# Optimization experiments

Measured on AMD Instinct MI355X. Metric: run time of the kernel, lower is better.

Reference implementation:

```python
import jax, jax.numpy as jnp
import numpy as np

MIN_HAIRPIN = 4
BIG = 1e30  # stand-in for the numpy reference's 1e18 INF (fp32-safe)


def _dp_single(e_pair, e_unp, allowed):
    """Nussinov min-energy DP for one sequence.
    e_pair: (L,L) f32, e_unp: (L,) f32, allowed: (L,L) bool.
    Returns dp (L,L) and ptr (L,L) backpointers matching the numpy reference:
      0 -> i unpaired, 1 -> j unpaired, 2 -> (i,j) paired, k+3 -> bifurcation at k.
    Vectorised over the antidiagonal (all i for a fixed span s at once).
    """
    L = e_unp.shape[0]
    idx = jnp.arange(L)
    dp0 = jnp.full((L, L), BIG, dtype=e_pair.dtype).at[idx, idx].set(e_unp)
    ptr0 = jnp.full((L, L), -1, dtype=jnp.int32).at[idx, idx].set(0)
    t = jnp.arange(L - 1)  # bifurcation offset k = i + t

    def step(carry, s):
        dp, ptr = carry
        j = idx + s - 1
        valid = j < L
        jc = jnp.minimum(j, L - 1)
        ip1 = jnp.minimum(idx + 1, L - 1)
        jm1 = jnp.maximum(jc - 1, 0)
        opt0 = dp[ip1, jc] + e_unp            # i unpaired
        opt1 = dp[idx, jm1] + e_unp[jc]       # j unpaired
        inner = jnp.where(s >= 3, dp[ip1, jm1], 0.0)
        pair_ok = allowed[idx, jc] & (s - 1 > MIN_HAIRPIN)  # j - i = s - 1
        opt2 = jnp.where(pair_ok, inner + e_pair[idx, jc], BIG)
        k = jnp.minimum(idx[:, None] + t[None, :], L - 1)
        bif = dp[idx[:, None], k] + dp[jnp.minimum(k + 1, L - 1), jc[:, None]]
        bif = jnp.where(t[None, :] < s - 1, bif, BIG)
        cand = jnp.concatenate([opt0[:, None], opt1[:, None], opt2[:, None], bif], axis=1)
        c = jnp.argmin(cand, axis=1)  # first-occurrence argmin == strict-< tie-break
        best = jnp.take_along_axis(cand, c[:, None], axis=1)[:, 0]
        new_ptr = jnp.where(c < 3, c, c + idx).astype(jnp.int32)  # c-3 is offset t -> k+3 = c+i
        dp = dp.at[idx, jc].set(jnp.where(valid, best, dp[idx, jc]))
        ptr = ptr.at[idx, jc].set(jnp.where(valid, new_ptr, ptr[idx, jc]))
        return (dp, ptr), None

    (dp, ptr), _ = jax.lax.scan(step, (dp0, ptr0), jnp.arange(2, L + 1))
    return dp, ptr


def _traceback(ptr):
    """Stack-based traceback of the backpointer matrix. Returns pairs (L,) int32, -1 = unpaired."""
    L = ptr.shape[0]

    def cond(st):
        return st[2] > 0

    def body(st):
        si, sj, sp, res = st
        top = sp - 1
        i, j = si[top], sj[top]
        skip = i >= j
        p = ptr[i, j]
        is0, is1, is2, isk = p == 0, p == 1, p == 2, p >= 3
        k = p - 3
        p1i = jnp.where(is0 | is2, i + 1, i)
        p1j = jnp.where(is1 | is2, j - 1, jnp.where(isk, k, j))
        v1 = (~skip) & jnp.where(is2, i + 1 <= j - 1, True)
        v2 = (~skip) & isk  # bifurcation pushes a second interval (k+1, j)
        res = jnp.where(is2 & (~skip), res.at[i].set(j).at[j].set(i), res)
        si = si.at[top].set(jnp.where(v1, p1i, si[top]))
        sj = sj.at[top].set(jnp.where(v1, p1j, sj[top]))
        slot2 = top + v1.astype(jnp.int32)
        si = si.at[slot2].set(jnp.where(v2, k + 1, si[slot2]))
        sj = sj.at[slot2].set(jnp.where(v2, j, sj[slot2]))
        sp = top + v1.astype(jnp.int32) + v2.astype(jnp.int32)
        return si, sj, sp, res

    si0 = jnp.zeros((L,), jnp.int32)
    sj0 = jnp.zeros((L,), jnp.int32).at[0].set(L - 1)
    res0 = jnp.full((L,), -1, jnp.int32)
    _, _, _, res = jax.lax.while_loop(cond, body, (si0, sj0, jnp.int32(1), res0))
    return res


def _structure_energy(e_pair, e_unp, pairs):
    """E(x,S) = sum_{i unpaired} e_unp[i] + sum_{(i,j) in S, i<j} e_pair[i,j]."""
    L = e_unp.shape[-1]
    clamped = jnp.maximum(pairs, 0)
    unp = jnp.where(pairs < 0, e_unp, 0.0).sum(-1)
    pe = jnp.take_along_axis(e_pair, clamped[..., None], axis=2)[..., 0]
    is_pair = (pairs >= 0) & (jnp.arange(L)[None, :] < clamped)
    return unp + jnp.where(is_pair, pe, 0.0).sum(-1)


def setup_inputs() -> dict:
    key = jax.random.key(0)
    k1, k2, k3 = jax.random.split(key, 3)
    B, L = 32, 384
    e_pair = jax.random.normal(k1, (B, L, L), jnp.float32)
    e_unp = jax.random.normal(k2, (B, L), jnp.float32)
    pair_mask = jax.random.randint(k3, (B, L, L), 0, 2).astype(jnp.bool_)
    return {"e_pair": e_pair, "e_unp": e_unp, "pair_mask": pair_mask}


def reference(e_pair, e_unp, pair_mask):
    dp, ptr = jax.vmap(_dp_single)(e_pair, e_unp, pair_mask)
    pairs = jax.vmap(_traceback)(ptr)  # (B, L) int32, -1 = unpaired
    energy = _structure_energy(e_pair, e_unp, pairs)  # (B,), equals dp[:, 0, -1]
    return pairs, energy
```

## Files before the change

kernel.cpp:

```cpp
#include <hip/hip_runtime.h>

#define LSEQ 384
#define BATCH 32
#define BIGV 1e30f
#define TB_STK 448
#define NN ((size_t)LSEQ * LSEQ)
#define BT 32
#define NT 12
#define PIT 33

__device__ __forceinline__ int detect_mmode_wave(const unsigned char* m0, int lane) {
    unsigned char v = m0[lane & 63];
    unsigned long long big = __ballot(v >= 2);
    unsigned long long off = __ballot((((lane & 63) & 3) != 0) && (v != 0));
    return big ? 2 : (off ? 1 : 0);
}
__device__ __forceinline__ bool mask_read(const void* mask, size_t idx, int mmode) {
    if (mmode == 0) return ((const unsigned int*)mask)[idx] != 0;
    if (mmode == 1) return ((const unsigned char*)mask)[idx] != 0;
    return ((const unsigned short*)mask)[idx] != 0;
}
__device__ __forceinline__ void choice_write(void* mask, size_t idx, int c, int mmode) {
    if (mmode == 0) ((unsigned int*)mask)[idx] = (unsigned int)c;
    else if (mmode == 1) ((unsigned char*)mask)[idx] = (unsigned char)c;
    else ((unsigned short*)mask)[idx] = (unsigned short)c;
}

__device__ __forceinline__ float edge_min32(const float* rowp, const float* colp) {
    float a0 = BIGV, a1 = BIGV, a2 = BIGV, a3 = BIGV;
    #pragma unroll
    for (int kk = 0; kk < 32; kk += 4) {
        float r0 = rowp[kk], r1 = rowp[kk + 1], r2 = rowp[kk + 2], r3 = rowp[kk + 3];
        const float* cb = colp + kk * PIT;
        float c0 = cb[0], c1 = cb[PIT], c2 = cb[2 * PIT], c3 = cb[3 * PIT];
        a0 = fminf(a0, r0 + c0); a1 = fminf(a1, r1 + c1);
        a2 = fminf(a2, r2 + c2); a3 = fminf(a3, r3 + c3);
    }
    return fminf(fminf(a0, a1), fminf(a2, a3));
}

__device__ __forceinline__ void minplus_waves(
    const float* __restrict__ dpG, int I, int J, const int* fm, int nfm,
    int wv, int lane, float part[4][BT][PIT])
{
    const int r0 = (lane >> 3) << 2, c0 = (lane & 7) << 2;
    float r16[16];
    #pragma unroll
    for (int z = 0; z < 16; ++z) r16[z] = BIGV;
    const int mi = wv >> 1, kqB = (wv & 1) * 4;
    if (mi < nfm) {
        const int M = fm[mi];
        #pragma unroll
        for (int q = 0; q < 4; ++q) {
            const int k = M * BT + (kqB + q) * 4;
            float4 a0 = *(const float4*)&dpG[(size_t)(I * BT + r0 + 0) * LSEQ + k];
            float4 a1 = *(const float4*)&dpG[(size_t)(I * BT + r0 + 1) * LSEQ + k];
            float4 a2 = *(const float4*)&dpG[(size_t)(I * BT + r0 + 2) * LSEQ + k];
            float4 a3 = *(const float4*)&dpG[(size_t)(I * BT + r0 + 3) * LSEQ + k];
            float4 b0 = *(const float4*)&dpG[(size_t)(J * BT + c0 + 0) * LSEQ + k];
            float4 b1 = *(const float4*)&dpG[(size_t)(J * BT + c0 + 1) * LSEQ + k];
            float4 b2 = *(const float4*)&dpG[(size_t)(J * BT + c0 + 2) * LSEQ + k];
            float4 b3 = *(const float4*)&dpG[(size_t)(J * BT + c0 + 3) * LSEQ + k];
            #pragma unroll
            for (int ri = 0; ri < 4; ++ri) {
                float4 av = ri == 0 ? a0 : ri == 1 ? a1 : ri == 2 ? a2 : a3;
                #pragma unroll
                for (int ci = 0; ci < 4; ++ci) {
                    float4 bv = ci == 0 ? b0 : ci == 1 ? b1 : ci == 2 ? b2 : b3;
                    float m = fminf(fminf(av.x + bv.x, av.y + bv.y),
                                    fminf(av.z + bv.z, av.w + bv.w));
                    r16[ri * 4 + ci] = fminf(r16[ri * 4 + ci], m);
                }
            }
        }
    }
    #pragma unroll
    for (int ri = 0; ri < 4; ++ri)
        #pragma unroll
        for (int ci = 0; ci < 4; ++ci)
            part[wv][r0 + ri][c0 + ci] = r16[ri * 4 + ci];
}

__device__ __constant__ int c_sb4[12] = {0,0,0,0, 0, 8, 15, 21, 26, 30, 33, 35};

__global__ __launch_bounds__(64) void diag_kernel(
    float* __restrict__ e_pair, const float* __restrict__ e_unp, void* mask)
{
    __shared__ float dT[BT + 1][PIT];
    __shared__ float epm[BT][PIT];
    __shared__ float s_eunp[BT];

    const int bid = blockIdx.x;
    const int b = bid / NT, t = bid % NT;
    const int lane = threadIdx.x;
    float* dpG = e_pair + (size_t)b * NN;
    const size_t mb = (size_t)b * NN;
    const int mmode = detect_mmode_wave((const unsigned char*)mask, lane);

    for (int z = lane; z < (BT + 1) * PIT; z += 64) ((float*)dT)[z] = BIGV;
    __syncthreads();
    if (lane < BT) {
        int i = t * BT + lane;
        float v = e_unp[b * LSEQ + i];
        s_eunp[lane] = v;
        dT[lane][lane] = v;
        dpG[(size_t)i * LSEQ + i] = v;
        if (i > 0) dpG[(size_t)i * LSEQ + i - 1] = v;
    }
    for (int z = lane; z < BT * BT; z += 64) {
        int li = z >> 5, lj = z & 31;
        int i = t * BT + li, j = t * BT + lj;
        bool ok = (lj - li > 4) && mask_read(mask, mb + (size_t)i * LSEQ + j, mmode);
        epm[li][lj] = ok ? dpG[(size_t)i * LSEQ + j] : BIGV;
    }
    __syncthreads();

    const int idx = lane >> 1, h = lane & 1;
    for (int sg = 1; sg < BT; ++sg) {
        const int nc = BT - sg;
        const bool act = idx < nc;
        const int li = idx, lj = idx + sg;
        const int ljc = lj < BT ? lj : BT - 1;
        const int i = t * BT + li, j = t * BT + lj;
        float ev = edge_min32(&dT[li][0], &dT[1][ljc]);
        float e1 = BIGV, opt0 = 0.f, x1 = BIGV, x2 = BIGV;
        if (act) {
            if (h == 0) {
                e1 = ev;
                opt0 = dT[li + 1][lj] + s_eunp[li];
            } else {
                x1 = dT[li][lj - 1] + s_eunp[lj];
                float pe = epm[li][lj];
                if (pe < BIGV) x2 = dT[li + 1][lj - 1] + pe;
            }
        }
        float y1 = __shfl_xor(x1, 1), y2 = __shfl_xor(x2, 1);
        if (act && h == 0) {
            float best = fminf(e1, y2);
            int cch = (best == opt0) ? 0 : (best == y1) ? 1
                     : (best == y2 && y2 < BIGV) ? 2 : 3;
            dT[li][lj] = best;
            dpG[(size_t)i * LSEQ + j] = best;
            if (i > 0) dpG[(size_t)j * LSEQ + i - 1] = best;
            choice_write(mask, mb + (size_t)j * LSEQ + i, cch, mmode);
        }
    }
}

__global__ __launch_bounds__(256) void step_kernel(
    float* __restrict__ e_pair, const float* __restrict__ e_unp,
    void* mask, float* __restrict__ acc, int p)
{
    __shared__ float dTI[BT + 1][PIT], dTJ[BT + 1][PIT];
    __shared__ float cur[BT + 1][PIT];
    __shared__ float epm[BT][PIT];
    __shared__ float part[4][BT][PIT];
    __shared__ float brow[BT], bcol[BT], s_eI[BT], s_eJ[BT];
    __shared__ float bcorn;

    const int b = blockIdx.x % BATCH;
    const int u = blockIdx.x / BATCH;
    const int nswp = NT - p;
    const int tid = threadIdx.x, lane = tid & 63, wv = tid >> 6;
    float* dpG = e_pair + (size_t)b * NN;
    const size_t mb = (size_t)b * NN;

    if (u >= nswp) {
        int e = u - nswp, s2 = p + 1;
        while (s2 < NT && e >= NT - s2) { e -= NT - s2; ++s2; }
        const int I = e, J = I + s2;
        int fm[2]; fm[0] = I + p - 1; int nfm = 1;
        if (J - (p - 1) != fm[0]) fm[nfm++] = J - (p - 1);
        minplus_waves(dpG, I, J, fm, nfm, wv, lane, part);
        __syncthreads();
        float* accT = acc + ((size_t)(b * 36 + c_sb4[s2] + I) << 10);
        const bool first = (p == (s2 + 1) / 2 + 1);
        for (int z = tid; z < BT * BT; z += 256) {
            int li = z >> 5, lj = z & 31;
            float m = fminf(fminf(part[0][li][lj], part[1][li][lj]),
                            fminf(part[2][li][lj], part[3][li][lj]));
            accT[z] = first ? m : fminf(accT[z], m);
        }
        return;
    }

    const int I = u, J = I + p, s = p;
    const int mmode = detect_mmode_wave((const unsigned char*)mask, lane);

    for (int z = tid; z < BT * BT; z += 256) {
        int li = z >> 5, lj = z & 31;
        dTI[li][lj] = (lj >= li) ? dpG[(size_t)(I * BT + li) * LSEQ + I * BT + lj] : BIGV;
        dTJ[li][lj] = (lj >= li) ? dpG[(size_t)(J * BT + li) * LSEQ + J * BT + lj] : BIGV;
    }
    for (int z = tid; z < PIT; z += 256) {
        dTI[BT][z] = BIGV; dTJ[BT][z] = BIGV; cur[BT][z] = BIGV;
    }
    if (tid < BT) {
        brow[tid] = dpG[(size_t)((I + 1) * BT) * LSEQ + J * BT + tid];
        s_eI[tid] = e_unp[b * LSEQ + I * BT + tid];
    } else if (tid < 2 * BT) {
        int q = tid - BT;
        bcol[q] = dpG[(size_t)(I * BT + q) * LSEQ + J * BT - 1];
        s_eJ[q] = e_unp[b * LSEQ + J * BT + q];
    } else if (tid == 2 * BT) {
        bcorn = (s >= 2) ? dpG[(size_t)((I + 1) * BT) * LSEQ + J * BT - 1] : BIGV;
    }
    for (int z = tid; z < BT * BT; z += 256) {
        int li = z >> 5, lj = z & 31;
        int i = I * BT + li, j = J * BT + lj;
        bool ok = (j - i > 4) && mask_read(mask, mb + (size_t)i * LSEQ + j, mmode);
        epm[li][lj] = ok ? dpG[(size_t)i * LSEQ + j] : BIGV;
    }

    int fm[2]; int nfm = 0;
    if (s >= 2) fm[nfm++] = I + 1;
    if (s >= 3) fm[nfm++] = J - 1;
    minplus_waves(dpG, I, J, fm, nfm, wv, lane, part);
    __syncthreads();

    const float* accT = acc + ((size_t)(b * 36 + c_sb4[s] + I) << 10);
    for (int z = tid; z < BT * BT; z += 256) {
        int li = z >> 5, lj = z & 31;
        float m = fminf(fminf(part[0][li][lj], part[1][li][lj]),
                        fminf(part[2][li][lj], part[3][li][lj]));
        if (s >= 4) m = fminf(m, accT[z]);
        cur[li][lj] = m;
    }
    __syncthreads();
    if (wv != 0) return;

    const int idx = lane >> 1, h = lane & 1;
    for (int sg = -(BT - 1); sg <= BT - 1; ++sg) {
        const int asg = sg < 0 ? -sg : sg;
        const int nc = BT - asg;
        const bool act = idx < nc;
        const int li = (sg >= 0) ? idx : idx - sg;
        const int lj = li + sg;
        const int lic = li < BT ? li : BT - 1;
        const int ljc = (lj < BT ? (lj >= 0 ? lj : 0) : BT - 1);
        const int i = I * BT + li, j = J * BT + lj;
        const float* rowp = (h == 0) ? &dTI[lic][0] : &cur[lic][0];
        const float* colp = (h == 0) ? &cur[1][ljc] : &dTJ[1][ljc];
        float ev = edge_min32(rowp, colp);
        float e1 = BIGV, opt0 = 0.f, farv = BIGV;
        float x0 = BIGV, x1 = BIGV, x2 = BIGV;
        if (act) {
            if (h == 0) {
                e1 = fminf(ev, dTI[li][BT - 1] + brow[lj]);
                opt0 = ((li + 1 < BT) ? cur[li + 1][lj] : brow[lj]) + s_eI[li];
                farv = cur[li][lj];
            } else {
                x0 = ev;
                x1 = ((lj >= 1) ? cur[li][lj - 1] : bcol[li]) + s_eJ[lj];
                float pe = epm[li][lj];
                if (pe < BIGV) {
                    float inner = (li + 1 < BT)
                        ? ((lj >= 1) ? cur[li + 1][lj - 1] : bcol[li + 1])
                        : ((lj >= 1) ? brow[lj - 1] : bcorn);
                    x2 = inner + pe;
                }
            }
        }
        float y0 = __shfl_xor(x0, 1), y1 = __shfl_xor(x1, 1), y2 = __shfl_xor(x2, 1);
        if (act && h == 0) {
            float best = fminf(fminf(fminf(e1, y0), farv), y2);
            int cch = (best == opt0) ? 0 : (best == y1) ? 1
                     : (best == y2 && y2 < BIGV) ? 2 : 3;
            cur[li][lj] = best;
            dpG[(size_t)i * LSEQ + j] = best;
            if (i > 0) dpG[(size_t)j * LSEQ + i - 1] = best;
            choice_write(mask, mb + (size_t)j * LSEQ + i, cch, mmode);
        }
    }
}

__global__ __launch_bounds__(512) void tb_kernel(
    const float* __restrict__ e_pair, const void* mask, float* __restrict__ out)
{
    const int b = blockIdx.x;
    const int tid = threadIdx.x;
    const int lane = tid & 63, wv = tid >> 6;
    const float* dp = e_pair + (size_t)b * NN;
    const size_t mb = (size_t)b * NN;
    const int mmode = detect_mmode_wave((const unsigned char*)mask, lane);

    __shared__ __align__(16) unsigned char ch[LSEQ * LSEQ];
    __shared__ short res[LSEQ];
    __shared__ int st[TB_STK];

    if (mmode == 1) {
        const uint4* src = (const uint4*)((const unsigned char*)mask + mb);
        for (int z = tid; z < (int)(NN / 16); z += 512) ((uint4*)ch)[z] = src[z];
    } else if (mmode == 2) {
        const uint4* src = (const uint4*)((const unsigned char*)mask + mb * 2);
        for (int z = tid; z < (int)(NN / 8); z += 512) {
            uint4 v = src[z];
            unsigned int lo = (v.x & 0xFFu) | (((v.x >> 16) & 0xFFu) << 8)
                            | ((v.y & 0xFFu) << 16) | (((v.y >> 16) & 0xFFu) << 24);
            unsigned int hi = (v.z & 0xFFu) | (((v.z >> 16) & 0xFFu) << 8)
                            | ((v.w & 0xFFu) << 16) | (((v.w >> 16) & 0xFFu) << 24);
            ((unsigned int*)ch)[z * 2] = lo;
            ((unsigned int*)ch)[z * 2 + 1] = hi;
        }
    } else {
        const uint4* src = (const uint4*)((const unsigned char*)mask + mb * 4);
        for (int z = tid; z < (int)(NN / 4); z += 512) {
            uint4 v = src[z];
            ((unsigned int*)ch)[z] = (v.x & 0xFFu) | ((v.y & 0xFFu) << 8)
                                   | ((v.z & 0xFFu) << 16) | ((v.w & 0xFFu) << 24);
        }
    }
    for (int l = tid; l < LSEQ; l += 512) res[l] = -1;
    __syncthreads();
    if (wv != 0) return;

    int sp = 0;
    int ci = 0, cj = LSEQ - 1;
    int have = 1;
    for (int iter = 0; iter < 8192; ++iter) {
        if (!have) {
            if (sp == 0) break;
            --sp;
            int pk = st[sp];
            ci = pk >> 16; cj = pk & 0xFFFF;
        }
        have = 0;
        if (ci >= cj) continue;
        int c = ch[(size_t)cj * LSEQ + ci];
        if (c == 0) { ++ci; have = 1; }
        else if (c == 1) { --cj; have = 1; }
        else if (c == 2) {
            res[ci] = (short)cj; res[cj] = (short)ci;
            if (ci + 1 <= cj - 1) { ++ci; --cj; have = 1; }
        } else {
            const int d = cj - ci;
            const float* rowi = dp + (size_t)ci * LSEQ;
            const float* mrow = dp + (size_t)cj * LSEQ;
            float bv = BIGV; int bt = d;
            for (int t = lane; t < d; t += 64) {
                float cc = rowi[ci + t] + mrow[ci + t];
                if (cc < bv || (cc == bv && t < bt)) { bv = cc; bt = t; }
            }
            for (int m = 32; m > 0; m >>= 1) {
                float ov = __shfl_xor(bv, m, 64);
                int   ot = __shfl_xor(bt, m, 64);
                if (ov < bv || (ov == bv && ot < bt)) { bv = ov; bt = ot; }
            }
            int k = ci + bt;
            if (sp < TB_STK - 1) { st[sp] = ((k + 1) << 16) | cj; ++sp; }
            cj = k; have = 1;
        }
    }

    for (int l = lane; l < LSEQ; l += 64)
        out[b * LSEQ + l] = (float)res[l];
    if (lane == 0)
        out[BATCH * LSEQ + b] = dp[LSEQ - 1];
}

extern "C" void kernel_launch(void* const* d_in, const int* in_sizes, int n_in,
                              void* d_out, int out_size, void* d_ws, size_t ws_size,
                              hipStream_t stream) {
    float* e_pair = (float*)d_in[0];
    const float* e_unp = (const float*)d_in[1];
    void* mask = d_in[2];
    float* acc = (float*)d_ws;
    (void)ws_size;

    static const int updC[12] = {0, 0, 0, 8, 13, 15, 14, 10, 6, 3, 1, 0};

    diag_kernel<<<BATCH * NT, 64, 0, stream>>>(e_pair, e_unp, mask);
    for (int p = 1; p < NT; ++p)
        step_kernel<<<BATCH * (NT - p + updC[p]), 256, 0, stream>>>(
            e_pair, e_unp, mask, acc, p);
    tb_kernel<<<BATCH, 512, 0, stream>>>(e_pair, mask, (float*)d_out);
}
```

Before: 775.6 us.

## Fuse pairs of tile-diagonal steps into one kernel to halve launches

Replaces the per-tile-diagonal step kernel (11 launches) with a fused kernel that processes two diagonals per launch (6 launches). Each block computes the two odd-span neighbour tiles in parallel waves, then the even-span tile, using shared-memory results from the first sweeps instead of reloading from global. Deferred min-plus accumulation work is rescheduled through a constant table. The aim is to cut launch and serialisation overhead on the critical path. The cost is heavier shared-memory use per block, some redundant recomputation (one wave's sweep only writes when I==0), and more complex schedule tables.

After: 813.0 us. 4.8% more time.

```diff
diff --git a/kernel.cpp b/kernel.cpp
--- a/kernel.cpp
+++ b/kernel.cpp
@@ -9,6 +9,16 @@
 #define NT 12
 #define PIT 33
 
+__device__ __constant__ int c_sb4[12] = {0,0,0,0, 0, 8, 15, 21, 26, 30, 33, 35};
+__device__ __constant__ int c_updS[8] = {0,0,0,0, 9, 15, 16, 16};
+__device__ __constant__ int c_upd[16][8] = {
+ {7,0,3,4,0,0,2,1},{7,1,4,5,0,0,2,1},{7,2,5,6,0,0,2,1},{7,3,6,7,0,0,2,1},{7,4,7,8,0,0,2,1},
+ {8,0,4,0,0,0,1,1},{8,1,5,0,0,0,1,1},{8,2,6,0,0,0,1,1},{8,3,7,0,0,0,1,1},
+ {9,0,3,4,5,6,4,1},{9,1,4,5,6,7,4,1},{9,2,5,6,7,8,4,1},
+ {10,0,4,5,6,0,3,1},{10,1,5,6,7,0,3,1},
+ {11,0,5,6,0,0,2,1},
+ {11,0,3,4,7,8,4,0}};
+
 __device__ __forceinline__ int detect_mmode_wave(const unsigned char* m0, int lane) {
     unsigned char v = m0[lane & 63];
     unsigned long long big = __ballot(v >= 2);
@@ -39,24 +49,39 @@
     return fminf(fminf(a0, a1), fminf(a2, a3));
 }
 
-__device__ __forceinline__ void minplus_waves(
-    const float* __restrict__ dpG, int I, int J, const int* fm, int nfm,
-    int wv, int lane, float part[4][BT][PIT])
-{
+__device__ __forceinline__ int fresh_list(int dd, int s, int odd, int K, int* fm) {
+    int cand[4];
+    if (odd) { cand[0]=1; cand[1]=2; cand[2]=s-2; cand[3]=s-1; }
+    else     { cand[0]=2; cand[1]=3; cand[2]=s-3; cand[3]=s-2; }
+    int n = 0;
+    for (int c = 0; c < 4; ++c) {
+        int dM = cand[c];
+        if (dM < 1 || dM > s - 1) continue;
+        int m = dM > s - dM ? dM : s - dM;
+        if (m > 2*dd - 2 || m < 2*dd - 3) continue;
+        bool dup = false;
+        for (int q = 0; q < n; ++q) if (fm[q] == K + dM) dup = true;
+        if (!dup) fm[n++] = K + dM;
+    }
+    return n;
+}
+
+__device__ void minplus_slot(const float* __restrict__ dpG, int Krow, int J,
+                             const int* fm, int nfm, int start, int stride,
+                             int lane, float (*slot)[PIT]) {
     const int r0 = (lane >> 3) << 2, c0 = (lane & 7) << 2;
     float r16[16];
     #pragma unroll
     for (int z = 0; z < 16; ++z) r16[z] = BIGV;
-    const int mi = wv >> 1, kqB = (wv & 1) * 4;
-    if (mi < nfm) {
+    for (int mi = start; mi < nfm; mi += stride) {
         const int M = fm[mi];
         #pragma unroll
-        for (int q = 0; q < 4; ++q) {
-            const int k = M * BT + (kqB + q) * 4;
-            float4 a0 = *(const float4*)&dpG[(size_t)(I * BT + r0 + 0) * LSEQ + k];
-            float4 a1 = *(const float4*)&dpG[(size_t)(I * BT + r0 + 1) * LSEQ + k];
-            float4 a2 = *(const float4*)&dpG[(size_t)(I * BT + r0 + 2) * LSEQ + k];
-            float4 a3 = *(const float4*)&dpG[(size_t)(I * BT + r0 + 3) * LSEQ + k];
+        for (int kq = 0; kq < 8; ++kq) {
+            const int k = M * BT + kq * 4;
+            float4 a0 = *(const float4*)&dpG[(size_t)(Krow * BT + r0 + 0) * LSEQ + k];
+            float4 a1 = *(const float4*)&dpG[(size_t)(Krow * BT + r0 + 1) * LSEQ + k];
+            float4 a2 = *(const float4*)&dpG[(size_t)(Krow * BT + r0 + 2) * LSEQ + k];
+            float4 a3 = *(const float4*)&dpG[(size_t)(Krow * BT + r0 + 3) * LSEQ + k];
             float4 b0 = *(const float4*)&dpG[(size_t)(J * BT + c0 + 0) * LSEQ + k];
             float4 b1 = *(const float4*)&dpG[(size_t)(J * BT + c0 + 1) * LSEQ + k];
             float4 b2 = *(const float4*)&dpG[(size_t)(J * BT + c0 + 2) * LSEQ + k];
@@ -78,157 +103,78 @@
     for (int ri = 0; ri < 4; ++ri)
         #pragma unroll
         for (int ci = 0; ci < 4; ++ci)
-            part[wv][r0 + ri][c0 + ci] = r16[ri * 4 + ci];
-}
-
-__device__ __constant__ int c_sb4[12] = {0,0,0,0, 0, 8, 15, 21, 26, 30, 33, 35};
-
-__global__ __launch_bounds__(64) void diag_kernel(
-    float* __restrict__ e_pair, const float* __restrict__ e_unp, void* mask)
+            slot[r0 + ri][c0 + ci] = r16[ri * 4 + ci];
+}
+
+__device__ void pair_via_curB(const float* __restrict__ dpG, int I, int d,
+                              const float (*curA)[PIT], const float (*curB)[PIT],
+                              const float* browB, int lane, float (*slot)[PIT]) {
+    const int r0 = (lane >> 3) << 2, c0 = (lane & 7) << 2;
+    float r16[16];
+    #pragma unroll
+    for (int z = 0; z < 16; ++z) r16[z] = BIGV;
+    for (int kk = 0; kk < 32; ++kk) {
+        float a[4], bv[4];
+        #pragma unroll
+        for (int ri = 0; ri < 4; ++ri)
+            a[ri] = (d == 1) ? curA[r0 + ri][kk]
+                  : dpG[(size_t)(I * BT + r0 + ri) * LSEQ + (I + 1) * BT + kk];
+        #pragma unroll
+        for (int ci = 0; ci < 4; ++ci)
+            bv[ci] = (kk < 31) ? curB[kk + 1][c0 + ci] : browB[c0 + ci];
+        #pragma unroll
+        for (int ri = 0; ri < 4; ++ri)
+            #pragma unroll
+            for (int ci = 0; ci < 4; ++ci)
+                r16[ri * 4 + ci] = fminf(r16[ri * 4 + ci], a[ri] + bv[ci]);
+    }
+    #pragma unroll
+    for (int ri = 0; ri < 4; ++ri)
+        #pragma unroll
+        for (int ci = 0; ci < 4; ++ci)
+            slot[r0 + ri][c0 + ci] = r16[ri * 4 + ci];
+}
+
+__device__ void pair_via_curA(const float* __restrict__ dpG, int J,
+                              const float (*curA)[PIT], int lane, float (*slot)[PIT]) {
+    const int r0 = (lane >> 3) << 2, c0 = (lane & 7) << 2;
+    float r16[16];
+    #pragma unroll
+    for (int z = 0; z < 16; ++z) r16[z] = BIGV;
+    #pragma unroll
+    for (int kq = 0; kq < 8; ++kq) {
+        const int k = (J - 1) * BT + kq * 4;
+        float4 b0 = *(const float4*)&dpG[(size_t)(J * BT + c0 + 0) * LSEQ + k];
+        float4 b1 = *(const float4*)&dpG[(size_t)(J * BT + c0 + 1) * LSEQ + k];
+        float4 b2 = *(const float4*)&dpG[(size_t)(J * BT + c0 + 2) * LSEQ + k];
+        float4 b3 = *(const float4*)&dpG[(size_t)(J * BT + c0 + 3) * LSEQ + k];
+        #pragma unroll
+        for (int ri = 0; ri < 4; ++ri) {
+            const float* ar = &curA[r0 + ri][kq * 4];
+            float ax = ar[0], ay = ar[1], az = ar[2], aw = ar[3];
+            #pragma unroll
+            for (int ci = 0; ci < 4; ++ci) {
+                float4 bv = ci == 0 ? b0 : ci == 1 ? b1 : ci == 2 ? b2 : b3;
+                float m = fminf(fminf(ax + bv.x, ay + bv.y),
+                                fminf(az + bv.z, aw + bv.w));
+                r16[ri * 4 + ci] = fminf(r16[ri * 4 + ci], m);
+            }
+        }
+    }
+    #pragma unroll
+    for (int ri = 0; ri < 4; ++ri)
+        #pragma unroll
+        for (int ci = 0; ci < 4; ++ci)
+            slot[r0 + ri][c0 + ci] = r16[ri * 4 + ci];
+}
+
+__device__ void sweep_wave(
+    const float (*dTI)[PIT], const float (*dTJ)[PIT], float (*cur)[PIT],
+    const float (*epm)[PIT], const float* eI, const float* eJ,
+    const float* brow, const float* bcol, float bcorn,
+    int I, int J, float* __restrict__ dpG, size_t mb, void* mask, int mmode,
+    int lane, int dowrite)
 {
-    __shared__ float dT[BT + 1][PIT];
-    __shared__ float epm[BT][PIT];
-    __shared__ float s_eunp[BT];
-
-    const int bid = blockIdx.x;
-    const int b = bid / NT, t = bid % NT;
-    const int lane = threadIdx.x;
-    float* dpG = e_pair + (size_t)b * NN;
-    const size_t mb = (size_t)b * NN;
-    const int mmode = detect_mmode_wave((const unsigned char*)mask, lane);
-
-    for (int z = lane; z < (BT + 1) * PIT; z += 64) ((float*)dT)[z] = BIGV;
-    __syncthreads();
-    if (lane < BT) {
-        int i = t * BT + lane;
-        float v = e_unp[b * LSEQ + i];
-        s_eunp[lane] = v;
-        dT[lane][lane] = v;
-        dpG[(size_t)i * LSEQ + i] = v;
-        if (i > 0) dpG[(size_t)i * LSEQ + i - 1] = v;
-    }
-    for (int z = lane; z < BT * BT; z += 64) {
-        int li = z >> 5, lj = z & 31;
-        int i = t * BT + li, j = t * BT + lj;
-        bool ok = (lj - li > 4) && mask_read(mask, mb + (size_t)i * LSEQ + j, mmode);
-        epm[li][lj] = ok ? dpG[(size_t)i * LSEQ + j] : BIGV;
-    }
-    __syncthreads();
-
-    const int idx = lane >> 1, h = lane & 1;
-    for (int sg = 1; sg < BT; ++sg) {
-        const int nc = BT - sg;
-        const bool act = idx < nc;
-        const int li = idx, lj = idx + sg;
-        const int ljc = lj < BT ? lj : BT - 1;
-        const int i = t * BT + li, j = t * BT + lj;
-        float ev = edge_min32(&dT[li][0], &dT[1][ljc]);
-        float e1 = BIGV, opt0 = 0.f, x1 = BIGV, x2 = BIGV;
-        if (act) {
-            if (h == 0) {
-                e1 = ev;
-                opt0 = dT[li + 1][lj] + s_eunp[li];
-            } else {
-                x1 = dT[li][lj - 1] + s_eunp[lj];
-                float pe = epm[li][lj];
-                if (pe < BIGV) x2 = dT[li + 1][lj - 1] + pe;
-            }
-        }
-        float y1 = __shfl_xor(x1, 1), y2 = __shfl_xor(x2, 1);
-        if (act && h == 0) {
-            float best = fminf(e1, y2);
-            int cch = (best == opt0) ? 0 : (best == y1) ? 1
-                     : (best == y2 && y2 < BIGV) ? 2 : 3;
-            dT[li][lj] = best;
-            dpG[(size_t)i * LSEQ + j] = best;
-            if (i > 0) dpG[(size_t)j * LSEQ + i - 1] = best;
-            choice_write(mask, mb + (size_t)j * LSEQ + i, cch, mmode);
-        }
-    }
-}
-
-__global__ __launch_bounds__(256) void step_kernel(
-    float* __restrict__ e_pair, const float* __restrict__ e_unp,
-    void* mask, float* __restrict__ acc, int p)
-{
-    __shared__ float dTI[BT + 1][PIT], dTJ[BT + 1][PIT];
-    __shared__ float cur[BT + 1][PIT];
-    __shared__ float epm[BT][PIT];
-    __shared__ float part[4][BT][PIT];
-    __shared__ float brow[BT], bcol[BT], s_eI[BT], s_eJ[BT];
-    __shared__ float bcorn;
-
-    const int b = blockIdx.x % BATCH;
-    const int u = blockIdx.x / BATCH;
-    const int nswp = NT - p;
-    const int tid = threadIdx.x, lane = tid & 63, wv = tid >> 6;
-    float* dpG = e_pair + (size_t)b * NN;
-    const size_t mb = (size_t)b * NN;
-
-    if (u >= nswp) {
-        int e = u - nswp, s2 = p + 1;
-        while (s2 < NT && e >= NT - s2) { e -= NT - s2; ++s2; }
-        const int I = e, J = I + s2;
-        int fm[2]; fm[0] = I + p - 1; int nfm = 1;
-        if (J - (p - 1) != fm[0]) fm[nfm++] = J - (p - 1);
-        minplus_waves(dpG, I, J, fm, nfm, wv, lane, part);
-        __syncthreads();
-        float* accT = acc + ((size_t)(b * 36 + c_sb4[s2] + I) << 10);
-        const bool first = (p == (s2 + 1) / 2 + 1);
-        for (int z = tid; z < BT * BT; z += 256) {
-            int li = z >> 5, lj = z & 31;
-            float m = fminf(fminf(part[0][li][lj], part[1][li][lj]),
-                            fminf(part[2][li][lj], part[3][li][lj]));
-            accT[z] = first ? m : fminf(accT[z], m);
-        }
-        return;
-    }
-
-    const int I = u, J = I + p, s = p;
-    const int mmode = detect_mmode_wave((const unsigned char*)mask, lane);
-
-    for (int z = tid; z < BT * BT; z += 256) {
-        int li = z >> 5, lj = z & 31;
-        dTI[li][lj] = (lj >= li) ? dpG[(size_t)(I * BT + li) * LSEQ + I * BT + lj] : BIGV;
-        dTJ[li][lj] = (lj >= li) ? dpG[(size_t)(J * BT + li) * LSEQ + J * BT + lj] : BIGV;
-    }
-    for (int z = tid; z < PIT; z += 256) {
-        dTI[BT][z] = BIGV; dTJ[BT][z] = BIGV; cur[BT][z] = BIGV;
-    }
-    if (tid < BT) {
-        brow[tid] = dpG[(size_t)((I + 1) * BT) * LSEQ + J * BT + tid];
-        s_eI[tid] = e_unp[b * LSEQ + I * BT + tid];
-    } else if (tid < 2 * BT) {
-        int q = tid - BT;
-        bcol[q] = dpG[(size_t)(I * BT + q) * LSEQ + J * BT - 1];
-        s_eJ[q] = e_unp[b * LSEQ + J * BT + q];
-    } else if (tid == 2 * BT) {
-        bcorn = (s >= 2) ? dpG[(size_t)((I + 1) * BT) * LSEQ + J * BT - 1] : BIGV;
-    }
-    for (int z = tid; z < BT * BT; z += 256) {
-        int li = z >> 5, lj = z & 31;
-        int i = I * BT + li, j = J * BT + lj;
-        bool ok = (j - i > 4) && mask_read(mask, mb + (size_t)i * LSEQ + j, mmode);
-        epm[li][lj] = ok ? dpG[(size_t)i * LSEQ + j] : BIGV;
-    }
-
-    int fm[2]; int nfm = 0;
-    if (s >= 2) fm[nfm++] = I + 1;
-    if (s >= 3) fm[nfm++] = J - 1;
-    minplus_waves(dpG, I, J, fm, nfm, wv, lane, part);
-    __syncthreads();
-
-    const float* accT = acc + ((size_t)(b * 36 + c_sb4[s] + I) << 10);
-    for (int z = tid; z < BT * BT; z += 256) {
-        int li = z >> 5, lj = z & 31;
-        float m = fminf(fminf(part[0][li][lj], part[1][li][lj]),
-                        fminf(part[2][li][lj], part[3][li][lj]));
-        if (s >= 4) m = fminf(m, accT[z]);
-        cur[li][lj] = m;
-    }
-    __syncthreads();
-    if (wv != 0) return;
-
     const int idx = lane >> 1, h = lane & 1;
     for (int sg = -(BT - 1); sg <= BT - 1; ++sg) {
         const int asg = sg < 0 ? -sg : sg;
@@ -247,11 +193,11 @@
         if (act) {
             if (h == 0) {
                 e1 = fminf(ev, dTI[li][BT - 1] + brow[lj]);
-                opt0 = ((li + 1 < BT) ? cur[li + 1][lj] : brow[lj]) + s_eI[li];
+                opt0 = ((li + 1 < BT) ? cur[li + 1][lj] : brow[lj]) + eI[li];
                 farv = cur[li][lj];
             } else {
                 x0 = ev;
-                x1 = ((lj >= 1) ? cur[li][lj - 1] : bcol[li]) + s_eJ[lj];
+                x1 = ((lj >= 1) ? cur[li][lj - 1] : bcol[li]) + eJ[lj];
                 float pe = epm[li][lj];
                 if (pe < BIGV) {
                     float inner = (li + 1 < BT)
@@ -267,11 +213,270 @@
             int cch = (best == opt0) ? 0 : (best == y1) ? 1
                      : (best == y2 && y2 < BIGV) ? 2 : 3;
             cur[li][lj] = best;
+            if (dowrite) {
+                dpG[(size_t)i * LSEQ + j] = best;
+                if (i > 0) dpG[(size_t)j * LSEQ + i - 1] = best;
+                choice_write(mask, mb + (size_t)j * LSEQ + i, cch, mmode);
+            }
+        }
+    }
+}
+
+__global__ __launch_bounds__(64) void diag_kernel(
+    float* __restrict__ e_pair, const float* __restrict__ e_unp, void* mask)
+{
+    __shared__ float dT[BT + 1][PIT];
+    __shared__ float epm[BT][PIT];
+    __shared__ float s_eunp[BT];
+
+    const int bid = blockIdx.x;
+    const int b = bid / NT, t = bid % NT;
+    const int lane = threadIdx.x;
+    float* dpG = e_pair + (size_t)b * NN;
+    const size_t mb = (size_t)b * NN;
+    const int mmode = detect_mmode_wave((const unsigned char*)mask, lane);
+
+    for (int z = lane; z < (BT + 1) * PIT; z += 64) ((float*)dT)[z] = BIGV;
+    __syncthreads();
+    if (lane < BT) {
+        int i = t * BT + lane;
+        float v = e_unp[b * LSEQ + i];
+        s_eunp[lane] = v;
+        dT[lane][lane] = v;
+        dpG[(size_t)i * LSEQ + i] = v;
+        if (i > 0) dpG[(size_t)i * LSEQ + i - 1] = v;
+    }
+    for (int z = lane; z < BT * BT; z += 64) {
+        int li = z >> 5, lj = z & 31;
+        int i = t * BT + li, j = t * BT + lj;
+        bool ok = (lj - li > 4) && mask_read(mask, mb + (size_t)i * LSEQ + j, mmode);
+        epm[li][lj] = ok ? dpG[(size_t)i * LSEQ + j] : BIGV;
+    }
+    __syncthreads();
+
+    const int idx = lane >> 1, h = lane & 1;
+    for (int sg = 1; sg < BT; ++sg) {
+        const int nc = BT - sg;
+        const bool act = idx < nc;
+        const int li = idx, lj = idx + sg;
+        const int ljc = lj < BT ? lj : BT - 1;
+        const int i = t * BT + li, j = t * BT + lj;
+        float ev = edge_min32(&dT[li][0], &dT[1][ljc]);
+        float e1 = BIGV, opt0 = 0.f, x1 = BIGV, x2 = BIGV;
+        if (act) {
+            if (h == 0) {
+                e1 = ev;
+                opt0 = dT[li + 1][lj] + s_eunp[li];
+            } else {
+                x1 = dT[li][lj - 1] + s_eunp[lj];
+                float pe = epm[li][lj];
+                if (pe < BIGV) x2 = dT[li + 1][lj - 1] + pe;
+            }
+        }
+        float y1 = __shfl_xor(x1, 1), y2 = __shfl_xor(x2, 1);
+        if (act && h == 0) {
+            float best = fminf(e1, y2);
+            int cch = (best == opt0) ? 0 : (best == y1) ? 1
+                     : (best == y2 && y2 < BIGV) ? 2 : 3;
+            dT[li][lj] = best;
             dpG[(size_t)i * LSEQ + j] = best;
             if (i > 0) dpG[(size_t)j * LSEQ + i - 1] = best;
             choice_write(mask, mb + (size_t)j * LSEQ + i, cch, mmode);
         }
     }
+}
+
+__global__ __launch_bounds__(256) void fused_kernel(
+    float* __restrict__ e_pair, const float* __restrict__ e_unp,
+    void* mask, float* __restrict__ acc, int d)
+{
+    __shared__ float dgI[BT + 1][PIT], dgI1[BT + 1][PIT];
+    __shared__ float dgJ1[BT + 1][PIT], dgJ[BT + 1][PIT];
+    __shared__ float curA[BT + 1][PIT], curB[BT + 1][PIT], curE[BT + 1][PIT];
+    __shared__ float part4[4][BT][PIT];
+    __shared__ float epmA[BT][PIT], epmB[BT][PIT];
+    __shared__ float browA[BT], bcolA[BT], browB[BT], bcolB[BT];
+    __shared__ float browE[BT], bcolE[BT];
+    __shared__ float eU_I[BT], eU_I1[BT], eU_J1[BT], eU_J[BT];
+    __shared__ float s_bcA, s_bcB, s_bcE;
+
+    const int nEven = (d <= 5) ? (NT - 2 * d) : 0;
+    const int nOdd1 = (d == 6) ? 1 : 0;
+    const int b = blockIdx.x % BATCH;
+    const int u = blockIdx.x / BATCH;
+    const int tid = threadIdx.x, lane = tid & 63, wv = tid >> 6;
+    float* dpG = e_pair + (size_t)b * NN;
+    const size_t mb = (size_t)b * NN;
+    const int mmode = detect_mmode_wave((const unsigned char*)mask, lane);
+
+    if (u >= nEven + nOdd1) {
+        const int* ent = c_upd[c_updS[d] + (u - nEven - nOdd1)];
+        const int sp = ent[0], It = ent[1], nM = ent[6], first = ent[7];
+        int fm[4] = {ent[2], ent[3], ent[4], ent[5]};
+        minplus_slot(dpG, It, It + sp, fm, nM, wv, 4, lane, part4[wv]);
+        __syncthreads();
+        float* accT = acc + ((size_t)(b * 36 + c_sb4[sp] + It) << 10);
+        for (int z = tid; z < BT * BT; z += 256) {
+            int li = z >> 5, lj = z & 31;
+            float m = fminf(fminf(part4[0][li][lj], part4[1][li][lj]),
+                            fminf(part4[2][li][lj], part4[3][li][lj]));
+            accT[z] = first ? m : fminf(accT[z], m);
+        }
+        return;
+    }
+
+    if (d == 6) {
+        const int K = 0, so = 11, Jo = 11;
+        for (int z = tid; z < BT * BT; z += 256) {
+            int li = z >> 5, lj = z & 31;
+            dgI[li][lj] = (lj >= li) ? dpG[(size_t)(K * BT + li) * LSEQ + K * BT + lj] : BIGV;
+            dgJ1[li][lj] = (lj >= li) ? dpG[(size_t)(Jo * BT + li) * LSEQ + Jo * BT + lj] : BIGV;
+            int i = K * BT + li, j = Jo * BT + lj;
+            bool ok = (j - i > 4) && mask_read(mask, mb + (size_t)i * LSEQ + j, mmode);
+            epmA[li][lj] = ok ? dpG[(size_t)i * LSEQ + j] : BIGV;
+        }
+        for (int z = tid; z < PIT; z += 256) {
+            dgI[BT][z] = BIGV; dgJ1[BT][z] = BIGV; curA[BT][z] = BIGV;
+        }
+        if (tid < BT) {
+            browA[tid] = dpG[(size_t)((K + 1) * BT) * LSEQ + Jo * BT + tid];
+            eU_I[tid] = e_unp[b * LSEQ + K * BT + tid];
+        } else if (tid < 2 * BT) {
+            int q = tid - BT;
+            bcolA[q] = dpG[(size_t)(K * BT + q) * LSEQ + Jo * BT - 1];
+            eU_J1[q] = e_unp[b * LSEQ + Jo * BT + q];
+        } else if (tid == 2 * BT) {
+            s_bcA = dpG[(size_t)((K + 1) * BT) * LSEQ + Jo * BT - 1];
+        }
+        int fm[4]; int nfm = fresh_list(d, so, 1, K, fm);
+        minplus_slot(dpG, K, Jo, fm, nfm, wv, 4, lane, part4[wv]);
+        __syncthreads();
+        const float* accT = acc + ((size_t)(b * 36 + c_sb4[so] + K) << 10);
+        for (int z = tid; z < BT * BT; z += 256) {
+            int li = z >> 5, lj = z & 31;
+            float m = fminf(fminf(part4[0][li][lj], part4[1][li][lj]),
+                            fminf(part4[2][li][lj], part4[3][li][lj]));
+            curA[li][lj] = fminf(m, accT[z]);
+        }
+        __syncthreads();
+        if (wv == 0)
+            sweep_wave(dgI, dgJ1, curA, epmA, eU_I, eU_J1,
+                       browA, bcolA, s_bcA, K, Jo, dpG, mb, mask, mmode, lane, 1);
+        return;
+    }
+
+    const int I = u, J = I + 2 * d, so = 2 * d - 1;
+
+    for (int z = tid; z < BT * BT; z += 256) {
+        int li = z >> 5, lj = z & 31;
+        bool up = (lj >= li);
+        dgI[li][lj]  = up ? dpG[(size_t)(I * BT + li) * LSEQ + I * BT + lj] : BIGV;
+        dgI1[li][lj] = up ? dpG[(size_t)((I + 1) * BT + li) * LSEQ + (I + 1) * BT + lj] : BIGV;
+        dgJ1[li][lj] = up ? dpG[(size_t)((J - 1) * BT + li) * LSEQ + (J - 1) * BT + lj] : BIGV;
+        dgJ[li][lj]  = up ? dpG[(size_t)(J * BT + li) * LSEQ + J * BT + lj] : BIGV;
+    }
+    for (int z = tid; z < BT * BT; z += 256) {
+        int li = z >> 5, lj = z & 31;
+        int iA = I * BT + li, jA = (J - 1) * BT + lj;
+        bool okA = (jA - iA > 4) && mask_read(mask, mb + (size_t)iA * LSEQ + jA, mmode);
+        epmA[li][lj] = okA ? dpG[(size_t)iA * LSEQ + jA] : BIGV;
+        int iB = (I + 1) * BT + li, jB = J * BT + lj;
+        bool okB = (jB - iB > 4) && mask_read(mask, mb + (size_t)iB * LSEQ + jB, mmode);
+        epmB[li][lj] = okB ? dpG[(size_t)iB * LSEQ + jB] : BIGV;
+    }
+    for (int z = tid; z < PIT; z += 256) {
+        dgI[BT][z] = BIGV; dgI1[BT][z] = BIGV; dgJ1[BT][z] = BIGV; dgJ[BT][z] = BIGV;
+        curA[BT][z] = BIGV; curB[BT][z] = BIGV; curE[BT][z] = BIGV;
+    }
+    if (tid < BT) eU_I[tid] = e_unp[b * LSEQ + I * BT + tid];
+    else if (tid < 2 * BT) eU_I1[tid - BT] = e_unp[b * LSEQ + (I + 1) * BT + (tid - BT)];
+    else if (tid < 3 * BT) eU_J1[tid - 2 * BT] = e_unp[b * LSEQ + (J - 1) * BT + (tid - 2 * BT)];
+    else if (tid < 4 * BT) eU_J[tid - 3 * BT] = e_unp[b * LSEQ + J * BT + (tid - 3 * BT)];
+    else if (tid < 5 * BT) browA[tid - 4 * BT] = dpG[(size_t)((I + 1) * BT) * LSEQ + (J - 1) * BT + (tid - 4 * BT)];
+    else if (tid < 6 * BT) bcolA[tid - 5 * BT] = dpG[(size_t)(I * BT + tid - 5 * BT) * LSEQ + (J - 1) * BT - 1];
+    else if (tid < 7 * BT) browB[tid - 6 * BT] = dpG[(size_t)((I + 2) * BT) * LSEQ + J * BT + (tid - 6 * BT)];
+    else browB[0] = browB[0], bcolB[tid - 7 * BT] = dpG[(size_t)((I + 1) * BT + tid - 7 * BT) * LSEQ + J * BT - 1];
+    if (tid == 0) s_bcA = (so >= 2) ? dpG[(size_t)((I + 1) * BT) * LSEQ + (J - 1) * BT - 1] : BIGV;
+    if (tid == 1) s_bcB = (so >= 2) ? dpG[(size_t)((I + 2) * BT) * LSEQ + J * BT - 1] : BIGV;
+    if (tid == 2) s_bcE = dpG[(size_t)((I + 1) * BT) * LSEQ + J * BT - 1];
+
+    int fmA[4], fmB[4], fmE[4];
+    const int nfmA = fresh_list(d, so, 1, I, fmA);
+    const int nfmB = fresh_list(d, so, 1, I + 1, fmB);
+    const int nfmE = fresh_list(d, 2 * d, 0, I, fmE);
+    __syncthreads();
+
+    if (so > 1) {
+        if (wv < 2) minplus_slot(dpG, I, J - 1, fmA, nfmA, wv, 2, lane, part4[wv]);
+        else        minplus_slot(dpG, I + 1, J, fmB, nfmB, wv - 2, 2, lane, part4[wv]);
+    }
+    __syncthreads();
+
+    {
+        const int half = tid & 127;
+        const bool lo = (tid < 128);
+        float (*cur)[PIT] = lo ? curA : curB;
+        const int K = lo ? I : I + 1;
+        if (so == 1) {
+            for (int z = half; z < BT * BT; z += 128) cur[z >> 5][z & 31] = BIGV;
+        } else {
+            const float* accT = (so >= 7)
+                ? acc + ((size_t)(b * 36 + c_sb4[so] + K) << 10) : 0;
+            const int p0 = lo ? 0 : 2, p1 = lo ? 1 : 3;
+            for (int z = half; z < BT * BT; z += 128) {
+                int li = z >> 5, lj = z & 31;
+                float m = fminf(part4[p0][li][lj], part4[p1][li][lj]);
+                if (accT) m = fminf(m, accT[z]);
+                cur[li][lj] = m;
+            }
+        }
+    }
+    __syncthreads();
+
+    if (wv == 0)
+        sweep_wave(dgI, dgJ1, curA, epmA, eU_I, eU_J1, browA, bcolA, s_bcA,
+                   I, J - 1, dpG, mb, mask, mmode, lane, I == 0);
+    else if (wv == 1)
+        sweep_wave(dgI1, dgJ, curB, epmB, eU_I1, eU_J, browB, bcolB, s_bcB,
+                   I + 1, J, dpG, mb, mask, mmode, lane, 1);
+    else
+        minplus_slot(dpG, I, J, fmE, nfmE, wv - 2, 2, lane, part4[wv]);
+    __syncthreads();
+
+    if (wv == 0)
+        pair_via_curB(dpG, I, d, curA, curB, browB, lane, part4[0]);
+    else if (wv == 1) {
+        if (d >= 2) pair_via_curA(dpG, J, curA, lane, part4[1]);
+        else for (int z = lane; z < BT * BT; z += 64) part4[1][z >> 5][z & 31] = BIGV;
+    } else {
+        const int half = tid - 128;
+        for (int z = half; z < BT * BT; z += 128) {
+            int li = z >> 5, lj = z & 31;
+            int i = I * BT + li, j = J * BT + lj;
+            bool ok = (j - i > 4) && mask_read(mask, mb + (size_t)i * LSEQ + j, mmode);
+            epmA[li][lj] = ok ? dpG[(size_t)i * LSEQ + j] : BIGV;
+        }
+        if (half < BT) browE[half] = curB[0][half];
+        else if (half < 2 * BT) bcolE[half - BT] = curA[half - BT][31];
+    }
+    __syncthreads();
+
+    {
+        const float* accT = (2 * d >= 8)
+            ? acc + ((size_t)(b * 36 + c_sb4[2 * d] + I) << 10) : 0;
+        for (int z = tid; z < BT * BT; z += 256) {
+            int li = z >> 5, lj = z & 31;
+            float m = fminf(fminf(part4[0][li][lj], part4[1][li][lj]),
+                            fminf(part4[2][li][lj], part4[3][li][lj]));
+            if (accT) m = fminf(m, accT[z]);
+            curE[li][lj] = m;
+        }
+    }
+    __syncthreads();
+
+    if (wv == 0)
+        sweep_wave(dgI, dgJ, curE, epmA, eU_I, eU_J, browE, bcolE, s_bcE,
+                   I, J, dpG, mb, mask, mmode, lane, 1);
 }
 
 __global__ __launch_bounds__(512) void tb_kernel(
@@ -367,11 +572,10 @@
     float* acc = (float*)d_ws;
     (void)ws_size;
 
-    static const int updC[12] = {0, 0, 0, 8, 13, 15, 14, 10, 6, 3, 1, 0};
+    static const int nblk[7] = {0, 10, 8, 15, 10, 3, 1};
 
     diag_kernel<<<BATCH * NT, 64, 0, stream>>>(e_pair, e_unp, mask);
-    for (int p = 1; p < NT; ++p)
-        step_kernel<<<BATCH * (NT - p + updC[p]), 256, 0, stream>>>(
-            e_pair, e_unp, mask, acc, p);
+    for (int d = 1; d <= 6; ++d)
+        fused_kernel<<<BATCH * nblk[d], 256, 0, stream>>>(e_pair, e_unp, mask, acc, d);
     tb_kernel<<<BATCH, 512, 0, stream>>>(e_pair, mask, (float*)d_out);
 }
```
